# Kernel tuning notes

Measured on AMD Instinct MI355X. Metric: run time of the kernel, lower is better.

The kernel has to match this reference:

```python
import jax, jax.numpy as jnp
import numpy as np

D = 768      # hidden_size
H = 12       # num_attention_heads
HD = D // H  # head_dim
B, S = 1, 4096


def setup_inputs() -> dict:
    key = jax.random.key(0)
    ks = jax.random.split(key, 9)
    s_in = 1.0 / np.sqrt(D)
    s_o = 1.0 / np.sqrt(D)
    x = jax.random.normal(ks[0], (B, S, D), dtype=jnp.float32)
    # per-head Q/K/V projections stacked: [H, D, HD]
    Wq = jax.random.uniform(ks[1], (H, D, HD), jnp.float32, -s_in, s_in)
    Wk = jax.random.uniform(ks[2], (H, D, HD), jnp.float32, -s_in, s_in)
    Wv = jax.random.uniform(ks[3], (H, D, HD), jnp.float32, -s_in, s_in)
    bq = jax.random.uniform(ks[4], (H, HD), jnp.float32, -s_in, s_in)
    bk = jax.random.uniform(ks[5], (H, HD), jnp.float32, -s_in, s_in)
    bv = jax.random.uniform(ks[6], (H, HD), jnp.float32, -s_in, s_in)
    Wo = jax.random.uniform(ks[7], (D, D), jnp.float32, -s_o, s_o)
    bo = jax.random.uniform(ks[8], (D,), jnp.float32, -s_o, s_o)
    return {"hidden_states": x, "Wq": Wq, "Wk": Wk, "Wv": Wv,
            "bq": bq, "bk": bk, "bv": bv, "Wo": Wo, "bo": bo}


def reference(hidden_states, Wq, Wk, Wv, bq, bk, bv, Wo, bo):
    x = hidden_states  # [B, S, D]
    # fused per-head projections -> [B, H, S, HD]
    q = jnp.einsum('bsd,hde->bhse', x, Wq) + bq[None, :, None, :]
    k = jnp.einsum('bsd,hde->bhse', x, Wk) + bk[None, :, None, :]
    v = jnp.einsum('bsd,hde->bhse', x, Wv) + bv[None, :, None, :]
    scale = 1.0 / jnp.sqrt(jnp.asarray(HD, q.dtype))
    scores = jnp.einsum('bhse,bhte->bhst', q, k) * scale  # [B, H, S, S]
    weights = jax.nn.softmax(scores, axis=-1)
    attn = jnp.einsum('bhst,bhte->bhse', weights, v)  # [B, H, S, HD]
    # concat heads along feature dim -> [B, S, D]
    concat = attn.transpose(0, 2, 1, 3).reshape(x.shape[0], x.shape[1], H * HD)
    return concat @ Wo + bo
```

## Files before the change

kernel.cpp:

```cpp
#include <hip/hip_runtime.h>

#define SLEN 4096
#define DMODEL 768
#define NH 12
#define HD 64
#define NQKV 2304
#define KDIM 768
#define KVBLK 64
#define NT (SLEN / KVBLK)

typedef _Float16 f16x8 __attribute__((ext_vector_type(8)));
typedef _Float16 f16x4v __attribute__((ext_vector_type(4)));
typedef float f32x4 __attribute__((ext_vector_type(4)));
typedef float f32x16 __attribute__((ext_vector_type(16)));

__device__ __forceinline__ void async16(void* lds, const void* g) {
  __builtin_amdgcn_global_load_lds((const __attribute__((address_space(1))) void*)g,
                                   (__attribute__((address_space(3))) void*)lds, 16, 0, 0);
}

__device__ __forceinline__ void plswap(unsigned& a, unsigned& b) {
  auto r = __builtin_amdgcn_permlane32_swap(a, b, false, false);
  a = r[0];
  b = r[1];
}

__device__ __forceinline__ unsigned pk(float a, float b) {
  auto r = __builtin_amdgcn_cvt_pkrtz(a, b);
  return __builtin_bit_cast(unsigned, r);
}

__global__ __launch_bounds__(256) void pack_kernel(
    const float* __restrict__ x, const float* __restrict__ Wq, const float* __restrict__ Wk,
    const float* __restrict__ Wv, const float* __restrict__ Wo,
    _Float16* __restrict__ xb, _Float16* __restrict__ wqkvt, _Float16* __restrict__ wot) {
  int tid = blockIdx.x * 256 + threadIdx.x;
  int stride = gridDim.x * 256;
  int n4 = SLEN * DMODEL / 4;
  for (int i = tid; i < n4; i += stride) {
    float4 v = ((const float4*)x)[i];
    f16x4v o = {(_Float16)v.x, (_Float16)v.y, (_Float16)v.z, (_Float16)v.w};
    ((f16x4v*)xb)[i] = o;
  }
  n4 = NQKV * DMODEL / 4;
  for (int i = tid; i < n4; i += stride) {
    int col = i / (DMODEL / 4);
    int d = (i - col * (DMODEL / 4)) * 4;
    int which = col / DMODEL;
    int cc = col - which * DMODEL;
    int h = cc >> 6, e = cc & 63;
    const float* W = which == 0 ? Wq : (which == 1 ? Wk : Wv);
    const float* s = W + (h * DMODEL + d) * HD + e;
    f16x4v o = {(_Float16)s[0], (_Float16)s[HD], (_Float16)s[2 * HD], (_Float16)s[3 * HD]};
    ((f16x4v*)wqkvt)[i] = o;
  }
  n4 = DMODEL * DMODEL / 4;
  for (int i = tid; i < n4; i += stride) {
    int o_ = i / (DMODEL / 4);
    int d = (i - o_ * (DMODEL / 4)) * 4;
    const float* s = Wo + d * DMODEL + o_;
    f16x4v o = {(_Float16)s[0], (_Float16)s[DMODEL], (_Float16)s[2 * DMODEL], (_Float16)s[3 * DMODEL]};
    ((f16x4v*)wot)[i] = o;
  }
}

__device__ __forceinline__ void gemm_core(const _Float16* __restrict__ A,
                                          const _Float16* __restrict__ Bt,
                                          _Float16* As, _Float16* Bs,
                                          f32x4 (&acc)[4][4], int m0, int n0) {
  int t = threadIdx.x;
  int lane = t & 63, w = t >> 6;
  int lr = lane & 15, lg = lane >> 4;
  int wr = w >> 1, wc = w & 1;
  for (int kb = 0; kb < KDIM / 64; ++kb) {
    #pragma unroll
    for (int i = 0; i < 4; ++i) {
      int base = (w * 4 + i) * 512;
      int off = base + lane * 8;
      int row = off >> 6, col = off & 63;
      async16(&As[base], A + (m0 + row) * KDIM + kb * 64 + col);
      async16(&Bs[base], Bt + (n0 + row) * KDIM + kb * 64 + col);
    }
    __syncthreads();
    #pragma unroll
    for (int kk = 0; kk < 2; ++kk) {
      f16x8 af[4], bf[4];
      #pragma unroll
      for (int mi = 0; mi < 4; ++mi)
        af[mi] = *(const f16x8*)&As[(wr * 64 + mi * 16 + lr) * 64 + kk * 32 + lg * 8];
      #pragma unroll
      for (int ni = 0; ni < 4; ++ni)
        bf[ni] = *(const f16x8*)&Bs[(wc * 64 + ni * 16 + lr) * 64 + kk * 32 + lg * 8];
      #pragma unroll
      for (int mi = 0; mi < 4; ++mi)
        #pragma unroll
        for (int ni = 0; ni < 4; ++ni)
          acc[mi][ni] = __builtin_amdgcn_mfma_f32_16x16x32_f16(af[mi], bf[ni], acc[mi][ni], 0, 0, 0);
    }
    __syncthreads();
  }
}

__global__ __launch_bounds__(256) void gemm_qkv(
    const _Float16* __restrict__ xb, const _Float16* __restrict__ wqkvt,
    const float* __restrict__ bq, const float* __restrict__ bk, const float* __restrict__ bv,
    _Float16* __restrict__ qd, _Float16* __restrict__ kd, _Float16* __restrict__ vtd) {
  __shared__ __align__(16) _Float16 As[128 * 64];
  __shared__ __align__(16) _Float16 Bs[128 * 64];
  f32x4 acc[4][4] = {};
  int m0 = blockIdx.y * 128, n0 = blockIdx.x * 128;
  gemm_core(xb, wqkvt, As, Bs, acc, m0, n0);
  int t = threadIdx.x, lane = t & 63, w = t >> 6;
  int lr = lane & 15, lg = lane >> 4;
  int wr = w >> 1, wc = w & 1;
  int which = n0 / DMODEL;
  const float* bias = which == 0 ? bq : (which == 1 ? bk : bv);
  #pragma unroll
  for (int mi = 0; mi < 4; ++mi)
    #pragma unroll
    for (int ni = 0; ni < 4; ++ni)
      #pragma unroll
      for (int r = 0; r < 4; ++r) {
        int srow = m0 + wr * 64 + mi * 16 + lg * 4 + r;
        int col = n0 + wc * 64 + ni * 16 + lr;
        int cc = col - which * DMODEL;
        int h = cc >> 6, e = cc & 63;
        float val = acc[mi][ni][r] + bias[cc];
        if (which < 2) {
          (which ? kd : qd)[h * (SLEN * HD) + srow * HD + e] = (_Float16)val;
        } else {
          vtd[h * (SLEN * HD) + e * SLEN + srow] = (_Float16)val;
        }
      }
}

__global__ __launch_bounds__(256, 5) void attn_kernel(
    const _Float16* __restrict__ qd, const _Float16* __restrict__ kd,
    const _Float16* __restrict__ vtd, _Float16* __restrict__ attn) {
  __shared__ __align__(16) _Float16 Ks[2][KVBLK * HD];
  __shared__ __align__(16) _Float16 Vts[2][HD * KVBLK];
  int wg = blockIdx.x;
  int orig = (wg & 7) * 96 + (wg >> 3);
  int qb = orig & 63, h = orig >> 6;
  int t = threadIdx.x, lane = t & 63, w = t >> 6;
  int wq = w & 1, wk = w >> 1;
  int ql = lane & 31, hi = lane >> 5;

  const _Float16* kbase = kd + h * (SLEN * HD);
  const _Float16* vbase = vtd + h * (SLEN * HD);

  auto stage = [&](int bi, int jb) {
    #pragma unroll
    for (int i = 0; i < 2; ++i) {
      int c = (w * 2 + i) * 64 + lane;
      int row = c >> 3;
      int sb = ((c & 7) * 16) ^ ((row & 7) << 4);
      async16(&Ks[bi][(w * 2 + i) * 512], kbase + (jb * KVBLK + row) * HD + sb / 2);
      async16(&Vts[bi][(w * 2 + i) * 512], vbase + row * SLEN + jb * KVBLK + sb / 2);
    }
  };

  int qrow = qb * 64 + wq * 32 + ql;
  const _Float16* qp = qd + h * (SLEN * HD) + qrow * HD;
  f16x8 qf[4];
  #pragma unroll
  for (int dblk = 0; dblk < 4; ++dblk)
    qf[dblk] = *(const f16x8*)(qp + dblk * 16 + hi * 8);

  f32x16 oacc[2] = {};
  float mrow = -1e30f, lrow = 0.f;
  const float C = 0.18033688f;
  const float THR = 44.4f;

  stage(0, 0);
  __syncthreads();
  int buf = 0;
  for (int jb = 0; jb < NT; ++jb) {
    if (jb + 1 < NT) stage(buf ^ 1, jb + 1);

    f32x16 sacc = {};
    __builtin_amdgcn_s_setprio(1);
    #pragma unroll
    for (int dblk = 0; dblk < 4; ++dblk) {
      int off = ((wk * 32 + ql) * 128 + dblk * 32 + hi * 16) ^ ((ql & 7) << 4);
      f16x8 kf = *(const f16x8*)((const char*)Ks[buf] + off);
      sacc = __builtin_amdgcn_mfma_f32_32x32x16_f16(kf, qf[dblk], sacc, 0, 0, 0);
    }
    __builtin_amdgcn_s_setprio(0);

    float mb = sacc[0];
    #pragma unroll
    for (int r = 1; r < 16; ++r) mb = fmaxf(mb, sacc[r]);
    {
      unsigned a = __builtin_bit_cast(unsigned, mb), b = a;
      plswap(a, b);
      mb = fmaxf(__builtin_bit_cast(float, a), __builtin_bit_cast(float, b));
    }
    if (!__all(mb <= mrow + THR)) {
      float mn = fmaxf(mrow, mb);
      float corr = __builtin_amdgcn_exp2f((mrow - mn) * C);
      lrow *= corr;
      #pragma unroll
      for (int r = 0; r < 16; ++r) { oacc[0][r] *= corr; oacc[1][r] *= corr; }
      mrow = mn;
    }
    float negm = -mrow * C;
    float p[16], ps = 0.f;
    #pragma unroll
    for (int r = 0; r < 16; ++r) { p[r] = __builtin_amdgcn_exp2f(fmaf(sacc[r], C, negm)); ps += p[r]; }
    lrow += ps;

    f16x8 pb[2];
    #pragma unroll
    for (int u = 0; u < 2; ++u) {
      unsigned a0 = pk(p[8 * u + 0], p[8 * u + 1]);
      unsigned b0 = pk(p[8 * u + 4], p[8 * u + 5]);
      unsigned a1 = pk(p[8 * u + 2], p[8 * u + 3]);
      unsigned b1 = pk(p[8 * u + 6], p[8 * u + 7]);
      plswap(a0, b0);
      plswap(a1, b1);
      union { unsigned wd[4]; f16x8 v; } uu;
      uu.wd[0] = a0; uu.wd[1] = a1; uu.wd[2] = b0; uu.wd[3] = b1;
      pb[u] = uu.v;
    }

    __builtin_amdgcn_s_setprio(1);
    #pragma unroll
    for (int u = 0; u < 2; ++u)
      #pragma unroll
      for (int eblk = 0; eblk < 2; ++eblk) {
        int off = ((eblk * 32 + ql) * 128 + wk * 64 + u * 32 + hi * 16) ^ ((ql & 7) << 4);
        f16x8 vf = *(const f16x8*)((const char*)Vts[buf] + off);
        oacc[eblk] = __builtin_amdgcn_mfma_f32_32x32x16_f16(vf, pb[u], oacc[eblk], 0, 0, 0);
      }
    __builtin_amdgcn_s_setprio(0);
    __syncthreads();
    buf ^= 1;
  }

  {
    unsigned a = __builtin_bit_cast(unsigned, lrow), b = a;
    plswap(a, b);
    lrow = __builtin_bit_cast(float, a) + __builtin_bit_cast(float, b);
  }

  float* Om = (float*)&Ks[0][0];
  float* Mm = (float*)&Vts[0][0];
  float* Lm = Mm + 64;
  if (wk == 1) {
    Mm[wq * 32 + ql] = mrow;
    Lm[wq * 32 + ql] = lrow;
    #pragma unroll
    for (int eblk = 0; eblk < 2; ++eblk)
      #pragma unroll
      for (int r = 0; r < 16; ++r) {
        int e = eblk * 32 + (r & 3) + 8 * (r >> 2) + 4 * hi;
        Om[(wq * 64 + e) * 32 + ql] = oacc[eblk][r];
      }
  }
  __syncthreads();
  if (wk == 0) {
    float m1 = Mm[wq * 32 + ql], l1 = Lm[wq * 32 + ql];
    float m = fmaxf(mrow, m1);
    float c0 = __builtin_amdgcn_exp2f((mrow - m) * C);
    float c1 = __builtin_amdgcn_exp2f((m1 - m) * C);
    float inv = 1.f / (lrow * c0 + l1 * c1);
    _Float16* ob = attn + qrow * DMODEL + h * HD;
    #pragma unroll
    for (int eblk = 0; eblk < 2; ++eblk) {
      float om[16];
      #pragma unroll
      for (int r = 0; r < 16; ++r) {
        int e = eblk * 32 + (r & 3) + 8 * (r >> 2) + 4 * hi;
        om[r] = (oacc[eblk][r] * c0 + Om[(wq * 64 + e) * 32 + ql] * c1) * inv;
      }
      #pragma unroll
      for (int i = 0; i < 4; ++i) {
        unsigned w0 = pk(om[4 * i + 0], om[4 * i + 1]);
        unsigned w1 = pk(om[4 * i + 2], om[4 * i + 3]);
        union { unsigned wd[2]; f16x4v v; } uu;
        uu.wd[0] = w0; uu.wd[1] = w1;
        *(f16x4v*)(ob + eblk * 32 + 8 * i + 4 * hi) = uu.v;
      }
    }
  }
}

__global__ __launch_bounds__(256) void gemm_out(
    const _Float16* __restrict__ attn, const _Float16* __restrict__ wot,
    const float* __restrict__ bo, float* __restrict__ out) {
  __shared__ __align__(16) _Float16 As[64 * 64];
  __shared__ __align__(16) _Float16 Bs[64 * 64];
  f32x4 acc[2][2] = {};
  int wg = blockIdx.x;
  int orig = (wg & 7) * 96 + (wg >> 3);
  int mb = orig / 12, nb = orig - mb * 12;
  int m0 = mb * 64, n0 = nb * 64;
  int t = threadIdx.x, lane = t & 63, w = t >> 6;
  int lr = lane & 15, lg = lane >> 4;
  int wr = w >> 1, wc = w & 1;
  for (int kb = 0; kb < KDIM / 64; ++kb) {
    #pragma unroll
    for (int i = 0; i < 2; ++i) {
      int base = (w * 2 + i) * 512;
      int off = base + lane * 8;
      int row = off >> 6, col = off & 63;
      async16(&As[base], attn + (m0 + row) * DMODEL + kb * 64 + col);
      async16(&Bs[base], wot + (n0 + row) * DMODEL + kb * 64 + col);
    }
    __syncthreads();
    #pragma unroll
    for (int kk = 0; kk < 2; ++kk) {
      f16x8 af[2], bf[2];
      #pragma unroll
      for (int mi = 0; mi < 2; ++mi)
        af[mi] = *(const f16x8*)&As[(wr * 32 + mi * 16 + lr) * 64 + kk * 32 + lg * 8];
      #pragma unroll
      for (int ni = 0; ni < 2; ++ni)
        bf[ni] = *(const f16x8*)&Bs[(wc * 32 + ni * 16 + lr) * 64 + kk * 32 + lg * 8];
      #pragma unroll
      for (int mi = 0; mi < 2; ++mi)
        #pragma unroll
        for (int ni = 0; ni < 2; ++ni)
          acc[mi][ni] = __builtin_amdgcn_mfma_f32_16x16x32_f16(af[mi], bf[ni], acc[mi][ni], 0, 0, 0);
    }
    __syncthreads();
  }
  #pragma unroll
  for (int mi = 0; mi < 2; ++mi)
    #pragma unroll
    for (int ni = 0; ni < 2; ++ni)
      #pragma unroll
      for (int r = 0; r < 4; ++r) {
        int srow = m0 + wr * 32 + mi * 16 + lg * 4 + r;
        int col = n0 + wc * 32 + ni * 16 + lr;
        out[srow * DMODEL + col] = acc[mi][ni][r] + bo[col];
      }
}

extern "C" void kernel_launch(void* const* d_in, const int* in_sizes, int n_in,
                              void* d_out, int out_size, void* d_ws, size_t ws_size,
                              hipStream_t stream) {
  const float* x  = (const float*)d_in[0];
  const float* Wq = (const float*)d_in[1];
  const float* Wk = (const float*)d_in[2];
  const float* Wv = (const float*)d_in[3];
  const float* bq = (const float*)d_in[4];
  const float* bk = (const float*)d_in[5];
  const float* bv = (const float*)d_in[6];
  const float* Wo = (const float*)d_in[7];
  const float* bo = (const float*)d_in[8];
  float* out = (float*)d_out;

  char* ws = (char*)d_ws;
  size_t off = 0;
  auto alloc = [&](size_t bytes) {
    char* p = ws + off;
    off += (bytes + 255) & ~size_t(255);
    return p;
  };
  _Float16* xb    = (_Float16*)alloc((size_t)SLEN * DMODEL * 2);
  _Float16* wqkvt = (_Float16*)alloc((size_t)NQKV * DMODEL * 2);
  _Float16* wot   = (_Float16*)alloc((size_t)DMODEL * DMODEL * 2);
  _Float16* qd    = (_Float16*)alloc((size_t)NH * SLEN * HD * 2);
  _Float16* kd    = (_Float16*)alloc((size_t)NH * SLEN * HD * 2);
  _Float16* vtd   = (_Float16*)alloc((size_t)NH * SLEN * HD * 2);
  _Float16* attn  = (_Float16*)alloc((size_t)SLEN * DMODEL * 2);

  hipLaunchKernelGGL(pack_kernel, dim3(1024), dim3(256), 0, stream,
                     x, Wq, Wk, Wv, Wo, xb, wqkvt, wot);
  hipLaunchKernelGGL(gemm_qkv, dim3(NQKV / 128, SLEN / 128), dim3(256), 0, stream,
                     xb, wqkvt, bq, bk, bv, qd, kd, vtd);
  hipLaunchKernelGGL(attn_kernel, dim3(768), dim3(256), 0, stream,
                     qd, kd, vtd, attn);
  hipLaunchKernelGGL(gemm_out, dim3(768), dim3(256), 0, stream,
                     attn, wot, bo, out);
}
```

Before: 237.0 us.

## Split attention over KV halves with merge kernel; retile QKV GEMM to 64x128

The attention kernel now divides the KV sequence into two splits per (head, q-block), which doubles the workgroup count to 1536 and gives better CU occupancy on a GPU with 256 CUs. Each split writes a partial normalized output plus its max and sum, and a new merge kernel combines the two partials into the final attn buffer. Separately, the QKV GEMM moves to 64x128 tiles with an XCD-aware swizzled 1D grid of 1152 blocks for more parallelism. The cost is an extra kernel launch, extra global traffic for the fp16 partials and stats, and a small loss of precision from storing the partials in fp16.

After: 232.9 us. No clear change (-1.7%).

```diff
diff --git a/kernel.cpp b/kernel.cpp
--- a/kernel.cpp
+++ b/kernel.cpp
@@ -64,65 +64,63 @@
   }
 }
 
-__device__ __forceinline__ void gemm_core(const _Float16* __restrict__ A,
-                                          const _Float16* __restrict__ Bt,
-                                          _Float16* As, _Float16* Bs,
-                                          f32x4 (&acc)[4][4], int m0, int n0) {
-  int t = threadIdx.x;
-  int lane = t & 63, w = t >> 6;
+__global__ __launch_bounds__(256, 5) void gemm_qkv(
+    const _Float16* __restrict__ xb, const _Float16* __restrict__ wqkvt,
+    const float* __restrict__ bq, const float* __restrict__ bk, const float* __restrict__ bv,
+    _Float16* __restrict__ qd, _Float16* __restrict__ kd, _Float16* __restrict__ vtd) {
+  __shared__ __align__(16) _Float16 As[64 * 64];
+  __shared__ __align__(16) _Float16 Bs[128 * 64];
+  int wg = blockIdx.x;
+  int orig = (wg & 7) * 144 + (wg >> 3);
+  int nb = orig % 18, mb = orig / 18;
+  int m0 = mb * 64, n0 = nb * 128;
+  int t = threadIdx.x, lane = t & 63, w = t >> 6;
   int lr = lane & 15, lg = lane >> 4;
-  int wr = w >> 1, wc = w & 1;
+  int wc = w;
+  f32x4 acc[4][2] = {};
   for (int kb = 0; kb < KDIM / 64; ++kb) {
+    #pragma unroll
+    for (int i = 0; i < 2; ++i) {
+      int base = (w * 2 + i) * 512;
+      int off = base + lane * 8;
+      int row = off >> 6, col = off & 63;
+      async16(&As[base], xb + (m0 + row) * KDIM + kb * 64 + col);
+    }
     #pragma unroll
     for (int i = 0; i < 4; ++i) {
       int base = (w * 4 + i) * 512;
       int off = base + lane * 8;
       int row = off >> 6, col = off & 63;
-      async16(&As[base], A + (m0 + row) * KDIM + kb * 64 + col);
-      async16(&Bs[base], Bt + (n0 + row) * KDIM + kb * 64 + col);
+      async16(&Bs[base], wqkvt + (n0 + row) * KDIM + kb * 64 + col);
     }
     __syncthreads();
     #pragma unroll
     for (int kk = 0; kk < 2; ++kk) {
-      f16x8 af[4], bf[4];
+      f16x8 af[4], bf[2];
       #pragma unroll
       for (int mi = 0; mi < 4; ++mi)
-        af[mi] = *(const f16x8*)&As[(wr * 64 + mi * 16 + lr) * 64 + kk * 32 + lg * 8];
-      #pragma unroll
-      for (int ni = 0; ni < 4; ++ni)
-        bf[ni] = *(const f16x8*)&Bs[(wc * 64 + ni * 16 + lr) * 64 + kk * 32 + lg * 8];
+        af[mi] = *(const f16x8*)&As[(mi * 16 + lr) * 64 + kk * 32 + lg * 8];
+      #pragma unroll
+      for (int ni = 0; ni < 2; ++ni)
+        bf[ni] = *(const f16x8*)&Bs[(wc * 32 + ni * 16 + lr) * 64 + kk * 32 + lg * 8];
       #pragma unroll
       for (int mi = 0; mi < 4; ++mi)
         #pragma unroll
-        for (int ni = 0; ni < 4; ++ni)
+        for (int ni = 0; ni < 2; ++ni)
           acc[mi][ni] = __builtin_amdgcn_mfma_f32_16x16x32_f16(af[mi], bf[ni], acc[mi][ni], 0, 0, 0);
     }
     __syncthreads();
   }
-}
-
-__global__ __launch_bounds__(256) void gemm_qkv(
-    const _Float16* __restrict__ xb, const _Float16* __restrict__ wqkvt,
-    const float* __restrict__ bq, const float* __restrict__ bk, const float* __restrict__ bv,
-    _Float16* __restrict__ qd, _Float16* __restrict__ kd, _Float16* __restrict__ vtd) {
-  __shared__ __align__(16) _Float16 As[128 * 64];
-  __shared__ __align__(16) _Float16 Bs[128 * 64];
-  f32x4 acc[4][4] = {};
-  int m0 = blockIdx.y * 128, n0 = blockIdx.x * 128;
-  gemm_core(xb, wqkvt, As, Bs, acc, m0, n0);
-  int t = threadIdx.x, lane = t & 63, w = t >> 6;
-  int lr = lane & 15, lg = lane >> 4;
-  int wr = w >> 1, wc = w & 1;
   int which = n0 / DMODEL;
   const float* bias = which == 0 ? bq : (which == 1 ? bk : bv);
   #pragma unroll
   for (int mi = 0; mi < 4; ++mi)
     #pragma unroll
-    for (int ni = 0; ni < 4; ++ni)
+    for (int ni = 0; ni < 2; ++ni)
       #pragma unroll
       for (int r = 0; r < 4; ++r) {
-        int srow = m0 + wr * 64 + mi * 16 + lg * 4 + r;
-        int col = n0 + wc * 64 + ni * 16 + lr;
+        int srow = m0 + mi * 16 + lg * 4 + r;
+        int col = n0 + wc * 32 + ni * 16 + lr;
         int cc = col - which * DMODEL;
         int h = cc >> 6, e = cc & 63;
         float val = acc[mi][ni][r] + bias[cc];
@@ -136,12 +134,16 @@
 
 __global__ __launch_bounds__(256, 5) void attn_kernel(
     const _Float16* __restrict__ qd, const _Float16* __restrict__ kd,
-    const _Float16* __restrict__ vtd, _Float16* __restrict__ attn) {
+    const _Float16* __restrict__ vtd, _Float16* __restrict__ Op, float* __restrict__ Ml,
+    int nsplit, int tilesper) {
   __shared__ __align__(16) _Float16 Ks[2][KVBLK * HD];
   __shared__ __align__(16) _Float16 Vts[2][HD * KVBLK];
   int wg = blockIdx.x;
-  int orig = (wg & 7) * 96 + (wg >> 3);
-  int qb = orig & 63, h = orig >> 6;
+  int nwg = 768 * nsplit;
+  int cpx = nwg >> 3;
+  int orig = (wg & 7) * cpx + (wg >> 3);
+  int s = orig % nsplit, u = orig / nsplit;
+  int qb = u & 63, h = u >> 6;
   int t = threadIdx.x, lane = t & 63, w = t >> 6;
   int wq = w & 1, wk = w >> 1;
   int ql = lane & 31, hi = lane >> 5;
@@ -172,11 +174,13 @@
   const float C = 0.18033688f;
   const float THR = 44.4f;
 
-  stage(0, 0);
+  int jb0 = s * tilesper;
+  stage(0, jb0);
   __syncthreads();
   int buf = 0;
-  for (int jb = 0; jb < NT; ++jb) {
-    if (jb + 1 < NT) stage(buf ^ 1, jb + 1);
+  for (int jj = 0; jj < tilesper; ++jj) {
+    int jb = jb0 + jj;
+    if (jj + 1 < tilesper) stage(buf ^ 1, jb + 1);
 
     f32x16 sacc = {};
     __builtin_amdgcn_s_setprio(1);
@@ -212,26 +216,26 @@
 
     f16x8 pb[2];
     #pragma unroll
-    for (int u = 0; u < 2; ++u) {
-      unsigned a0 = pk(p[8 * u + 0], p[8 * u + 1]);
-      unsigned b0 = pk(p[8 * u + 4], p[8 * u + 5]);
-      unsigned a1 = pk(p[8 * u + 2], p[8 * u + 3]);
-      unsigned b1 = pk(p[8 * u + 6], p[8 * u + 7]);
+    for (int u2 = 0; u2 < 2; ++u2) {
+      unsigned a0 = pk(p[8 * u2 + 0], p[8 * u2 + 1]);
+      unsigned b0 = pk(p[8 * u2 + 4], p[8 * u2 + 5]);
+      unsigned a1 = pk(p[8 * u2 + 2], p[8 * u2 + 3]);
+      unsigned b1 = pk(p[8 * u2 + 6], p[8 * u2 + 7]);
       plswap(a0, b0);
       plswap(a1, b1);
       union { unsigned wd[4]; f16x8 v; } uu;
       uu.wd[0] = a0; uu.wd[1] = a1; uu.wd[2] = b0; uu.wd[3] = b1;
-      pb[u] = uu.v;
+      pb[u2] = uu.v;
     }
 
     __builtin_amdgcn_s_setprio(1);
     #pragma unroll
-    for (int u = 0; u < 2; ++u)
+    for (int u2 = 0; u2 < 2; ++u2)
       #pragma unroll
       for (int eblk = 0; eblk < 2; ++eblk) {
-        int off = ((eblk * 32 + ql) * 128 + wk * 64 + u * 32 + hi * 16) ^ ((ql & 7) << 4);
+        int off = ((eblk * 32 + ql) * 128 + wk * 64 + u2 * 32 + hi * 16) ^ ((ql & 7) << 4);
         f16x8 vf = *(const f16x8*)((const char*)Vts[buf] + off);
-        oacc[eblk] = __builtin_amdgcn_mfma_f32_32x32x16_f16(vf, pb[u], oacc[eblk], 0, 0, 0);
+        oacc[eblk] = __builtin_amdgcn_mfma_f32_32x32x16_f16(vf, pb[u2], oacc[eblk], 0, 0, 0);
       }
     __builtin_amdgcn_s_setprio(0);
     __syncthreads();
@@ -264,8 +268,14 @@
     float m = fmaxf(mrow, m1);
     float c0 = __builtin_amdgcn_exp2f((mrow - m) * C);
     float c1 = __builtin_amdgcn_exp2f((m1 - m) * C);
-    float inv = 1.f / (lrow * c0 + l1 * c1);
-    _Float16* ob = attn + qrow * DMODEL + h * HD;
+    float ltot = lrow * c0 + l1 * c1;
+    float inv = 1.f / ltot;
+    int q = wq * 32 + ql;
+    if (hi == 0) {
+      Ml[orig * 128 + q] = m;
+      Ml[orig * 128 + 64 + q] = ltot;
+    }
+    _Float16* ob = Op + (size_t)orig * 4096 + q * 64;
     #pragma unroll
     for (int eblk = 0; eblk < 2; ++eblk) {
       float om[16];
@@ -283,6 +293,34 @@
         *(f16x4v*)(ob + eblk * 32 + 8 * i + 4 * hi) = uu.v;
       }
     }
+  }
+}
+
+__global__ __launch_bounds__(256) void merge_kernel(
+    const _Float16* __restrict__ Op, const float* __restrict__ Ml,
+    _Float16* __restrict__ attn, int nsplit) {
+  const float C = 0.18033688f;
+  int u = blockIdx.x;
+  int qb = u & 63, h = u >> 6;
+  int t = threadIdx.x;
+  int e = t & 63, qg = t >> 6;
+  for (int j = 0; j < 16; ++j) {
+    int q = qg * 16 + j;
+    float out;
+    if (nsplit == 2) {
+      int i0 = u * 2, i1 = u * 2 + 1;
+      float m0 = Ml[i0 * 128 + q], l0 = Ml[i0 * 128 + 64 + q];
+      float m1 = Ml[i1 * 128 + q], l1 = Ml[i1 * 128 + 64 + q];
+      float m = fmaxf(m0, m1);
+      float w0 = l0 * __builtin_amdgcn_exp2f((m0 - m) * C);
+      float w1 = l1 * __builtin_amdgcn_exp2f((m1 - m) * C);
+      float v0 = (float)Op[(size_t)i0 * 4096 + q * 64 + e];
+      float v1 = (float)Op[(size_t)i1 * 4096 + q * 64 + e];
+      out = (v0 * w0 + v1 * w1) / (w0 + w1);
+    } else {
+      out = (float)Op[(size_t)u * 4096 + q * 64 + e];
+    }
+    attn[(size_t)(qb * 64 + q) * DMODEL + h * HD + e] = (_Float16)out;
   }
 }
 
@@ -367,12 +405,20 @@
   _Float16* vtd   = (_Float16*)alloc((size_t)NH * SLEN * HD * 2);
   _Float16* attn  = (_Float16*)alloc((size_t)SLEN * DMODEL * 2);
 
+  size_t need2 = ((size_t)1536 * 4096 * 2 + 255 + (size_t)1536 * 128 * 4 + 255);
+  int nsplit = (ws_size >= off + need2) ? 2 : 1;
+  int nunits = 768 * nsplit;
+  _Float16* Op = (_Float16*)alloc((size_t)nunits * 4096 * 2);
+  float*    Mlb = (float*)alloc((size_t)nunits * 128 * 4);
+
   hipLaunchKernelGGL(pack_kernel, dim3(1024), dim3(256), 0, stream,
                      x, Wq, Wk, Wv, Wo, xb, wqkvt, wot);
-  hipLaunchKernelGGL(gemm_qkv, dim3(NQKV / 128, SLEN / 128), dim3(256), 0, stream,
+  hipLaunchKernelGGL(gemm_qkv, dim3(1152), dim3(256), 0, stream,
                      xb, wqkvt, bq, bk, bv, qd, kd, vtd);
-  hipLaunchKernelGGL(attn_kernel, dim3(768), dim3(256), 0, stream,
-                     qd, kd, vtd, attn);
+  hipLaunchKernelGGL(attn_kernel, dim3(nunits), dim3(256), 0, stream,
+                     qd, kd, vtd, Op, Mlb, nsplit, NT / nsplit);
+  hipLaunchKernelGGL(merge_kernel, dim3(768), dim3(256), 0, stream,
+                     Op, Mlb, attn, nsplit);
   hipLaunchKernelGGL(gemm_out, dim3(768), dim3(256), 0, stream,
                      attn, wot, bo, out);
 }
```
